# Kernel tuning notes

Measured on AMD Instinct MI355X. Metric: run time of the kernel, lower is better.

The kernel has to match this reference:

```python
import jax, jax.numpy as jnp
import numpy as np

N, M, D = 8192, 8192, 512

def setup_inputs() -> dict:
    key = jax.random.key(0)
    kx, ky = jax.random.split(key)
    X = jax.random.normal(kx, (N, D), dtype=jnp.float32)
    Y = jax.random.normal(ky, (M, D), dtype=jnp.float32)
    gamma = jnp.float32(1.0)  # learnable scalar kernel width
    return {"X": X, "Y": Y, "gamma": gamma}

def reference(X, Y, gamma):
    # RBF kernel: exp(-gamma * ||x_i - y_j||^2)
    x2 = jnp.sum(X * X, axis=-1)            # [n]
    y2 = jnp.sum(Y * Y, axis=-1)            # [m]
    xy = jnp.einsum('nd,md->nm', X, Y)      # [n, m] GEMM
    sq = x2[:, None] + y2[None, :] - 2.0 * xy
    sq = jnp.maximum(sq, 0.0)               # clamp tiny negatives from fp error
    return jnp.exp(-gamma * sq)
```

## Files before the change

kernel.cpp:

```cpp
#include <hip/hip_runtime.h>
#include <hip/hip_bf16.h>


#define NROWS 8192
#define D_DIM 512
#define BM 256
#define BN 256
#define BK 64
#define NKT (D_DIM / BK)

using bf16x8 = __attribute__((ext_vector_type(8))) short;
using f32x4  = __attribute__((ext_vector_type(4))) float;

__device__ inline unsigned pack2_bf16(float a, float b) {
    unsigned ua = __builtin_bit_cast(unsigned, a);
    unsigned ub = __builtin_bit_cast(unsigned, b);
    ua = (ua + 0x7fffu + ((ua >> 16) & 1u)) >> 16;
    ub = (ub + 0x7fffu + ((ub >> 16) & 1u)) >> 16;
    return ua | (ub << 16);
}

__global__ __launch_bounds__(64) void prep_kernel(const float* __restrict__ src,
                                                  unsigned short* __restrict__ dst,
                                                  float* __restrict__ norms) {
    const int row  = blockIdx.x;
    const int lane = threadIdx.x;
    const float4* s = reinterpret_cast<const float4*>(src) + (size_t)row * (D_DIM / 4);
    float4 v0 = s[lane * 2];
    float4 v1 = s[lane * 2 + 1];
    float ss = v0.x * v0.x + v0.y * v0.y + v0.z * v0.z + v0.w * v0.w +
               v1.x * v1.x + v1.y * v1.y + v1.z * v1.z + v1.w * v1.w;
    uint4 p;
    p.x = pack2_bf16(v0.x, v0.y);
    p.y = pack2_bf16(v0.z, v0.w);
    p.z = pack2_bf16(v1.x, v1.y);
    p.w = pack2_bf16(v1.z, v1.w);
    reinterpret_cast<uint4*>(dst + (size_t)row * D_DIM)[lane] = p;
    #pragma unroll
    for (int off = 32; off; off >>= 1) ss += __shfl_down(ss, off);
    if (lane == 0) norms[row] = ss;
}

__device__ inline void gload_lds16(const unsigned short* g, unsigned short* l) {
    __builtin_amdgcn_global_load_lds(
        (const __attribute__((address_space(1))) void*)g,
        (__attribute__((address_space(3))) void*)l, 16, 0, 0);
}

__global__ __launch_bounds__(512, 2) void rbf_gemm(
    const unsigned short* __restrict__ Xb, const unsigned short* __restrict__ Yb,
    const float* __restrict__ x2, const float* __restrict__ y2,
    const float* __restrict__ gptr, float* __restrict__ out) {
    __shared__ unsigned short sA[2][BM * BK];
    __shared__ unsigned short sB[2][BN * BK];

    const int bid  = blockIdx.x;
    const int swz  = (bid & 7) * 128 + (bid >> 3);
    const int brow = swz >> 5;
    const int bcol = swz & 31;

    const int tid  = threadIdx.x;
    const int lane = tid & 63;
    const int wid  = tid >> 6;
    const int wr   = wid >> 2;
    const int wc   = wid & 3;

    const int srow = tid >> 3;
    const int scol = ((tid & 7) ^ ((tid >> 3) & 7)) * 8;
    const unsigned short* gA0 = Xb + (size_t)(brow * BM) * D_DIM + scol;
    const unsigned short* gB0 = Yb + (size_t)(bcol * BN) * D_DIM + scol;

    const int lr = lane & 15;
    const int kg = lane >> 4;
    const int lx = lane & 7;
    const int sl0 = ((0 * 4 + kg) ^ lx) * 8;
    const int sl1 = ((1 * 4 + kg) ^ lx) * 8;
    const int aBase = (wr * 128 + lr) * BK;
    const int bBase = (wc * 64 + lr) * BK;

    f32x4 acc[8][4] = {};
    bf16x8 av[4][2], bv[4][2];

    auto STAGE = [&](int d, int kt, int q) {
        const bool isA = q >= 2;
        const int half = q & 1;
        const unsigned short* g = (isA ? gA0 : gB0) +
            (size_t)(half * 128 + srow) * D_DIM + kt * BK;
        unsigned short* l = (isA ? sA[d] : sB[d]) +
            (half * 128 + srow) * BK + (tid & 7) * 8;
        gload_lds16(g, l);
        gload_lds16(g + 64 * D_DIM, l + 64 * BK);
    };

    #define LDF(p) (*reinterpret_cast<const bf16x8*>(p))
    #define MFMA(a, b, c) __builtin_amdgcn_mfma_f32_16x16x32_bf16(a, b, c, 0, 0, 0)

    #pragma unroll
    for (int q = 0; q < 4; ++q) STAGE(0, 0, q);

    for (int t = 0; t < NKT; ++t) {
        const int c = t & 1, d = c ^ 1;
        const bool pre = (t + 1 < NKT);
        const unsigned short* A = sA[c];
        const unsigned short* B = sB[c];

        if (pre) STAGE(d, t + 1, 0);
        if (pre) asm volatile("s_waitcnt vmcnt(2)" ::: "memory");
        else     asm volatile("s_waitcnt vmcnt(0)" ::: "memory");
        asm volatile("s_barrier" ::: "memory");
        #pragma unroll
        for (int m = 0; m < 4; ++m) {
            av[m][0] = LDF(A + aBase + m * 16 * BK + sl0);
            av[m][1] = LDF(A + aBase + m * 16 * BK + sl1);
        }
        #pragma unroll
        for (int n = 0; n < 2; ++n) {
            bv[n][0] = LDF(B + bBase + n * 16 * BK + sl0);
            bv[n][1] = LDF(B + bBase + n * 16 * BK + sl1);
        }
        __builtin_amdgcn_s_setprio(1);
        #pragma unroll
        for (int m = 0; m < 4; ++m)
            #pragma unroll
            for (int n = 0; n < 2; ++n) {
                acc[m][n] = MFMA(av[m][0], bv[n][0], acc[m][n]);
                acc[m][n] = MFMA(av[m][1], bv[n][1], acc[m][n]);
            }
        __builtin_amdgcn_s_setprio(0);
        asm volatile("s_barrier" ::: "memory");

        if (pre) STAGE(d, t + 1, 1);
        #pragma unroll
        for (int n = 2; n < 4; ++n) {
            bv[n][0] = LDF(B + bBase + n * 16 * BK + sl0);
            bv[n][1] = LDF(B + bBase + n * 16 * BK + sl1);
        }
        __builtin_amdgcn_s_setprio(1);
        #pragma unroll
        for (int m = 0; m < 4; ++m)
            #pragma unroll
            for (int n = 2; n < 4; ++n) {
                acc[m][n] = MFMA(av[m][0], bv[n][0], acc[m][n]);
                acc[m][n] = MFMA(av[m][1], bv[n][1], acc[m][n]);
            }
        __builtin_amdgcn_s_setprio(0);
        asm volatile("s_barrier" ::: "memory");

        if (pre) STAGE(d, t + 1, 2);
        #pragma unroll
        for (int m = 0; m < 4; ++m) {
            av[m][0] = LDF(A + aBase + (m + 4) * 16 * BK + sl0);
            av[m][1] = LDF(A + aBase + (m + 4) * 16 * BK + sl1);
        }
        __builtin_amdgcn_s_setprio(1);
        #pragma unroll
        for (int m = 0; m < 4; ++m)
            #pragma unroll
            for (int n = 0; n < 2; ++n) {
                acc[m + 4][n] = MFMA(av[m][0], bv[n][0], acc[m + 4][n]);
                acc[m + 4][n] = MFMA(av[m][1], bv[n][1], acc[m + 4][n]);
            }
        __builtin_amdgcn_s_setprio(0);
        asm volatile("s_barrier" ::: "memory");

        if (pre) STAGE(d, t + 1, 3);
        __builtin_amdgcn_s_setprio(1);
        #pragma unroll
        for (int m = 0; m < 4; ++m)
            #pragma unroll
            for (int n = 2; n < 4; ++n) {
                acc[m + 4][n] = MFMA(av[m][0], bv[n][0], acc[m + 4][n]);
                acc[m + 4][n] = MFMA(av[m][1], bv[n][1], acc[m + 4][n]);
            }
        __builtin_amdgcn_s_setprio(0);
        asm volatile("s_barrier" ::: "memory");
    }

    const float g = *gptr;
    const int rbase = brow * BM + wr * 128 + (kg << 2);
    const int cbase = bcol * BN + wc * 64 + lr;

    float yv[4];
    #pragma unroll
    for (int n = 0; n < 4; ++n) yv[n] = y2[cbase + n * 16];

    #pragma unroll
    for (int m = 0; m < 8; ++m) {
        #pragma unroll
        for (int r = 0; r < 4; ++r) {
            const float xr = x2[rbase + m * 16 + r];
            const size_t ro = (size_t)(rbase + m * 16 + r) * NROWS + cbase;
            #pragma unroll
            for (int n = 0; n < 4; ++n) {
                float sq = fmaxf(xr + yv[n] - 2.0f * acc[m][n][r], 0.0f);
                out[ro + n * 16] = __expf(-g * sq);
            }
        }
    }
}

extern "C" void kernel_launch(void* const* d_in, const int* in_sizes, int n_in,
                              void* d_out, int out_size, void* d_ws, size_t ws_size,
                              hipStream_t stream) {
    const float* X = (const float*)d_in[0];
    const float* Y = (const float*)d_in[1];
    const float* gamma = (const float*)d_in[2];
    float* out = (float*)d_out;

    unsigned short* Xb = (unsigned short*)d_ws;
    unsigned short* Yb = Xb + (size_t)NROWS * D_DIM;
    float* x2 = (float*)(Yb + (size_t)NROWS * D_DIM);
    float* y2 = x2 + NROWS;

    prep_kernel<<<NROWS, 64, 0, stream>>>(X, Xb, x2);
    prep_kernel<<<NROWS, 64, 0, stream>>>(Y, Yb, y2);

    const int grid = (NROWS / BM) * (NROWS / BN);
    rbf_gemm<<<grid, 512, 0, stream>>>(Xb, Yb, x2, y2, gamma, out);
}
```

Before: 364.8 us.

## Restructure staging order to match consumption and use nontemporal output stores

Reorders the staging of the next K tile so the A and B quarter-tiles are issued in the order they are consumed, with the B-tile row mapping changed to match. Vmcnt waits are placed just before the barrier of the phase that needs the data, which lets LDS reads of the current tile overlap with in-flight global-to-LDS loads and drops a barrier per iteration. The epilogue now writes output with nontemporal stores to avoid polluting caches with the large output. The finer wait-count accounting risks races if the counts or barriers are wrong.

```diff
diff --git a/kernel.cpp b/kernel.cpp
--- a/kernel.cpp
+++ b/kernel.cpp
@@ -47,6 +47,11 @@
         (__attribute__((address_space(3))) void*)l, 16, 0, 0);
 }
 
+#define VMCNT(n) asm volatile("s_waitcnt vmcnt(" #n ")" ::: "memory")
+#define BAR()    asm volatile("s_barrier" ::: "memory")
+#define LDF(p)   (*reinterpret_cast<const bf16x8*>(p))
+#define MFMA(a, b, c) __builtin_amdgcn_mfma_f32_16x16x32_bf16(a, b, c, 0, 0, 0)
+
 __global__ __launch_bounds__(512, 2) void rbf_gemm(
     const unsigned short* __restrict__ Xb, const unsigned short* __restrict__ Yb,
     const float* __restrict__ x2, const float* __restrict__ y2,
@@ -65,14 +70,31 @@
     const int wr   = wid >> 2;
     const int wc   = wid & 3;
 
-    const int srow = tid >> 3;
-    const int scol = ((tid & 7) ^ ((tid >> 3) & 7)) * 8;
-    const unsigned short* gA0 = Xb + (size_t)(brow * BM) * D_DIM + scol;
-    const unsigned short* gB0 = Yb + (size_t)(bcol * BN) * D_DIM + scol;
-
-    const int lr = lane & 15;
-    const int kg = lane >> 4;
-    const int lx = lane & 7;
+    const int slot  = tid & 7;
+    const int srowA = tid >> 3;
+    const int srowB = ((tid >> 3) & 31) + ((tid >> 8) << 6);
+    const int scol  = (slot ^ ((tid >> 3) & 7)) * 8;
+    const unsigned short* gA = Xb + (size_t)(brow * BM + srowA) * D_DIM + scol;
+    const unsigned short* gB = Yb + (size_t)(bcol * BN + srowB) * D_DIM + scol;
+    const int loffA = srowA * BK + slot * 8;
+    const int loffB = srowB * BK + slot * 8;
+
+    auto stA = [&](int d, int kt, int odd) {
+        const unsigned short* g = gA + (size_t)(odd * 64) * D_DIM + kt * BK;
+        unsigned short* l = sA[d] + odd * 64 * BK + loffA;
+        gload_lds16(g, l);
+        gload_lds16(g + 128 * D_DIM, l + 128 * BK);
+    };
+    auto stB = [&](int d, int kt, int odd) {
+        const unsigned short* g = gB + (size_t)(odd * 32) * D_DIM + kt * BK;
+        unsigned short* l = sB[d] + odd * 32 * BK + loffB;
+        gload_lds16(g, l);
+        gload_lds16(g + 128 * D_DIM, l + 128 * BK);
+    };
+
+    const int lr  = lane & 15;
+    const int kg  = lane >> 4;
+    const int lx  = lane & 7;
     const int sl0 = ((0 * 4 + kg) ^ lx) * 8;
     const int sl1 = ((1 * 4 + kg) ^ lx) * 8;
     const int aBase = (wr * 128 + lr) * BK;
@@ -81,22 +103,9 @@
     f32x4 acc[8][4] = {};
     bf16x8 av[4][2], bv[4][2];
 
-    auto STAGE = [&](int d, int kt, int q) {
-        const bool isA = q >= 2;
-        const int half = q & 1;
-        const unsigned short* g = (isA ? gA0 : gB0) +
-            (size_t)(half * 128 + srow) * D_DIM + kt * BK;
-        unsigned short* l = (isA ? sA[d] : sB[d]) +
-            (half * 128 + srow) * BK + (tid & 7) * 8;
-        gload_lds16(g, l);
-        gload_lds16(g + 64 * D_DIM, l + 64 * BK);
-    };
-
-    #define LDF(p) (*reinterpret_cast<const bf16x8*>(p))
-    #define MFMA(a, b, c) __builtin_amdgcn_mfma_f32_16x16x32_bf16(a, b, c, 0, 0, 0)
-
-    #pragma unroll
-    for (int q = 0; q < 4; ++q) STAGE(0, 0, q);
+    stA(0, 0, 0); stB(0, 0, 0); stB(0, 0, 1); stA(0, 0, 1);
+    VMCNT(4);
+    BAR();
 
     for (int t = 0; t < NKT; ++t) {
         const int c = t & 1, d = c ^ 1;
@@ -104,10 +113,6 @@
         const unsigned short* A = sA[c];
         const unsigned short* B = sB[c];
 
-        if (pre) STAGE(d, t + 1, 0);
-        if (pre) asm volatile("s_waitcnt vmcnt(2)" ::: "memory");
-        else     asm volatile("s_waitcnt vmcnt(0)" ::: "memory");
-        asm volatile("s_barrier" ::: "memory");
         #pragma unroll
         for (int m = 0; m < 4; ++m) {
             av[m][0] = LDF(A + aBase + m * 16 * BK + sl0);
@@ -118,6 +123,9 @@
             bv[n][0] = LDF(B + bBase + n * 16 * BK + sl0);
             bv[n][1] = LDF(B + bBase + n * 16 * BK + sl1);
         }
+        if (pre) { stA(d, t + 1, 0); VMCNT(4); }
+        else     { VMCNT(2); }
+        BAR();
         __builtin_amdgcn_s_setprio(1);
         #pragma unroll
         for (int m = 0; m < 4; ++m)
@@ -127,14 +135,15 @@
                 acc[m][n] = MFMA(av[m][1], bv[n][1], acc[m][n]);
             }
         __builtin_amdgcn_s_setprio(0);
-        asm volatile("s_barrier" ::: "memory");
-
-        if (pre) STAGE(d, t + 1, 1);
+
         #pragma unroll
         for (int n = 2; n < 4; ++n) {
             bv[n][0] = LDF(B + bBase + n * 16 * BK + sl0);
             bv[n][1] = LDF(B + bBase + n * 16 * BK + sl1);
         }
+        if (pre) { stB(d, t + 1, 0); VMCNT(4); }
+        else     { VMCNT(0); }
+        BAR();
         __builtin_amdgcn_s_setprio(1);
         #pragma unroll
         for (int m = 0; m < 4; ++m)
@@ -144,14 +153,14 @@
                 acc[m][n] = MFMA(av[m][1], bv[n][1], acc[m][n]);
             }
         __builtin_amdgcn_s_setprio(0);
-        asm volatile("s_barrier" ::: "memory");
-
-        if (pre) STAGE(d, t + 1, 2);
+
         #pragma unroll
         for (int m = 0; m < 4; ++m) {
             av[m][0] = LDF(A + aBase + (m + 4) * 16 * BK + sl0);
             av[m][1] = LDF(A + aBase + (m + 4) * 16 * BK + sl1);
         }
+        if (pre) stB(d, t + 1, 1);
+        BAR();
         __builtin_amdgcn_s_setprio(1);
         #pragma unroll
         for (int m = 0; m < 4; ++m)
@@ -161,9 +170,12 @@
                 acc[m + 4][n] = MFMA(av[m][1], bv[n][1], acc[m + 4][n]);
             }
         __builtin_amdgcn_s_setprio(0);
-        asm volatile("s_barrier" ::: "memory");
-
-        if (pre) STAGE(d, t + 1, 3);
+
+        if (pre) {
+            stA(d, t + 1, 1);
+            VMCNT(4);
+            BAR();
+        }
         __builtin_amdgcn_s_setprio(1);
         #pragma unroll
         for (int m = 0; m < 4; ++m)
@@ -173,7 +185,6 @@
                 acc[m + 4][n] = MFMA(av[m][1], bv[n][1], acc[m + 4][n]);
             }
         __builtin_amdgcn_s_setprio(0);
-        asm volatile("s_barrier" ::: "memory");
     }
 
     const float g = *gptr;
@@ -193,7 +204,7 @@
             #pragma unroll
             for (int n = 0; n < 4; ++n) {
                 float sq = fmaxf(xr + yv[n] - 2.0f * acc[m][n][r], 0.0f);
-                out[ro + n * 16] = __expf(-g * sq);
+                __builtin_nontemporal_store(__expf(-g * sq), &out[ro + n * 16]);
             }
         }
     }
```

Measured after the change: 355.8 us. 1.03x faster.
